# Optimization experiments

Measured on AMD Instinct MI355X. Metric: run time of the kernel, lower is better.

The kernel has to match this reference:

```python
import jax, jax.numpy as jnp
import numpy as np

N = 100000   # nodes
E = 1600000  # edges (avg degree 16)
F = 128      # num_features
H = 128      # hidden_channels
C = 8        # num_classes


def _gcn_conv(x, src, dst, W, b, num_nodes):
    """PyG GCNConv: add self-loops, symmetric normalization, linear-then-aggregate, +bias."""
    h = x @ W  # [N, out]
    loops = jnp.arange(num_nodes, dtype=src.dtype)
    s = jnp.concatenate([src, loops])
    d = jnp.concatenate([dst, loops])
    deg = jax.ops.segment_sum(jnp.ones_like(s, dtype=h.dtype), d, num_segments=num_nodes)
    dinv = jax.lax.rsqrt(jnp.maximum(deg, 1.0))  # deg >= 1 thanks to self-loops
    norm = dinv[s] * dinv[d]  # [E+N]
    out = jax.ops.segment_sum(h[s] * norm[:, None], d, num_segments=num_nodes)
    return out + b


def setup_inputs() -> dict:
    key = jax.random.key(0)
    k1, k2, k3, k4 = jax.random.split(key, 4)
    x = jax.random.normal(k1, (N, F), dtype=jnp.float32)
    edge_index = jax.random.randint(k2, (2, E), 0, N, dtype=jnp.int32)
    W1 = jax.random.normal(k3, (F, H), dtype=jnp.float32) * (1.0 / np.sqrt(F))
    b1 = jnp.zeros((H,), dtype=jnp.float32)
    W2 = jax.random.normal(k4, (H, C), dtype=jnp.float32) * (1.0 / np.sqrt(H))
    b2 = jnp.zeros((C,), dtype=jnp.float32)
    return {"x": x, "edge_index": edge_index, "W1": W1, "b1": b1, "W2": W2, "b2": b2}


def reference(x, edge_index, W1, b1, W2, b2):
    src, dst = edge_index[0], edge_index[1]
    h = _gcn_conv(x, src, dst, W1, b1, N)
    h = jax.nn.relu(h)
    out = _gcn_conv(h, src, dst, W2, b2, N)
    return out
```

## Files before the change

kernel.cpp:

```cpp
#include <hip/hip_runtime.h>
#include <hip/hip_bf16.h>
#include <hip/hip_fp16.h>

#define NN 100000
#define EE 1600000
#define FF 128
#define HH 128
#define CC 8

#define CH 4096
#define NBK ((NN + 511) / 512)
#define NCH ((EE + CH - 1) / CH)
#define HSZ (NBK * NCH)

typedef _Float16 half8 __attribute__((ext_vector_type(8)));
typedef float f32x4 __attribute__((ext_vector_type(4)));

__global__ __launch_bounds__(1024) void k_scan1(const int* __restrict__ in,
                                                int* __restrict__ outp,
                                                int* __restrict__ bsum, int n) {
  __shared__ int sh[1024];
  int t = threadIdx.x;
  int i = blockIdx.x * 1024 + t;
  int v = (i < n) ? in[i] : 0;
  sh[t] = v;
  __syncthreads();
  for (int offs = 1; offs < 1024; offs <<= 1) {
    int add = (t >= offs) ? sh[t - offs] : 0;
    __syncthreads();
    sh[t] += add;
    __syncthreads();
  }
  if (i < n) outp[i] = sh[t] - v;
  if (t == 1023) bsum[blockIdx.x] = sh[1023];
}

__global__ __launch_bounds__(128) void k_scan2(int* __restrict__ bsum, int nb) {
  __shared__ int sh[128];
  int t = threadIdx.x;
  int v = (t < nb) ? bsum[t] : 0;
  sh[t] = v;
  __syncthreads();
  for (int offs = 1; offs < 128; offs <<= 1) {
    int add = (t >= offs) ? sh[t - offs] : 0;
    __syncthreads();
    sh[t] += add;
    __syncthreads();
  }
  if (t < nb) bsum[t] = sh[t] - v;
}

__global__ __launch_bounds__(1024) void k_scan3(int* __restrict__ outp,
                                                const int* __restrict__ bsum,
                                                int n, int e) {
  int i = blockIdx.x * 1024 + threadIdx.x;
  if (i < n) outp[i] += bsum[blockIdx.x];
  if (i == 0) outp[n] = e;
}

__global__ __launch_bounds__(256) void k_histA(const int* __restrict__ dst,
                                               int* __restrict__ hist) {
  __shared__ int lh[NBK];
  int c = blockIdx.x, t = threadIdx.x;
  for (int b = t; b < NBK; b += 256) lh[b] = 0;
  __syncthreads();
  int e0 = c * CH, e1 = min(e0 + CH, EE);
  for (int j = e0 + t; j < e1; j += 256) atomicAdd(&lh[dst[j] >> 9], 1);
  __syncthreads();
  for (int b = t; b < NBK; b += 256) hist[b * NCH + c] = lh[b];
}

__global__ __launch_bounds__(256) void k_scatA(const int* __restrict__ src,
                                               const int* __restrict__ dst,
                                               const int* __restrict__ hoff,
                                               unsigned int* __restrict__ stage) {
  __shared__ int lcur[NBK];
  int c = blockIdx.x, t = threadIdx.x;
  for (int b = t; b < NBK; b += 256) lcur[b] = hoff[b * NCH + c];
  __syncthreads();
  int e0 = c * CH, e1 = min(e0 + CH, EE);
  for (int j = e0 + t; j < e1; j += 256) {
    int d = dst[j];
    int pos = atomicAdd(&lcur[d >> 9], 1);
    stage[pos] = (unsigned int)src[j] | ((unsigned int)(d & 511) << 17);
  }
}

__global__ __launch_bounds__(256) void k_bucketB(const unsigned int* __restrict__ stage,
                                                 const int* __restrict__ hoff,
                                                 int* __restrict__ col,
                                                 int* __restrict__ rowptr,
                                                 float* __restrict__ dinv) {
  __shared__ int lcnt[512];
  __shared__ int lpart[256];
  int b = blockIdx.x, t = threadIdx.x;
  int n0 = b * 512;
  lcnt[t] = 0;
  lcnt[t + 256] = 0;
  __syncthreads();
  int e0 = hoff[b * NCH];
  int e1 = hoff[(b + 1) * NCH];
  for (int j = e0 + t; j < e1; j += 256)
    atomicAdd(&lcnt[stage[j] >> 17], 1);
  __syncthreads();
  int c0 = lcnt[2 * t], c1 = lcnt[2 * t + 1];
  lpart[t] = c0 + c1;
  __syncthreads();
  for (int offs = 1; offs < 256; offs <<= 1) {
    int add = (t >= offs) ? lpart[t - offs] : 0;
    __syncthreads();
    lpart[t] += add;
    __syncthreads();
  }
  int base0 = e0 + lpart[t] - (c0 + c1);
  int base1 = base0 + c0;
  int node0 = n0 + 2 * t, node1 = n0 + 2 * t + 1;
  if (node0 <= NN) rowptr[node0] = base0;
  if (node1 <= NN) rowptr[node1] = base1;
  if (node0 < NN) dinv[node0] = rsqrtf((float)c0 + 1.f);
  if (node1 < NN) dinv[node1] = rsqrtf((float)c1 + 1.f);
  lcnt[2 * t] = base0;
  lcnt[2 * t + 1] = base1;
  __syncthreads();
  for (int j = e0 + t; j < e1; j += 256) {
    unsigned int v = stage[j];
    int pos = atomicAdd(&lcnt[v >> 17], 1);
    col[pos] = (int)(v & 0x1FFFFu);
  }
}

__global__ __launch_bounds__(256) void k_gemm1(const float* __restrict__ x,
                                               const float* __restrict__ W,
                                               __half* __restrict__ h, int n) {
  __shared__ _Float16 Wl[128 * 128];
  int t = threadIdx.x;
  {
    int c = t & 127;
    int kg0 = t >> 7;
    for (int kg = kg0; kg < 16; kg += 2) {
      _Float16 tmp[8];
#pragma unroll
      for (int j = 0; j < 8; ++j)
        tmp[j] = (_Float16)W[(size_t)(kg * 8 + j) * 128 + c];
      int byteoff = (c * 256 + kg * 16) ^ ((c & 7) << 4);
      *(half8*)((char*)Wl + byteoff) = *(half8*)tmp;
    }
  }
  __syncthreads();

  int row0 = blockIdx.x * 64;
  int w = t >> 6, l = t & 63;
  int rw = w >> 1, cw = w & 1;
  int lr = l & 15, g = l >> 4;

  f32x4 acc[2][4];
#pragma unroll
  for (int ar = 0; ar < 2; ++ar)
#pragma unroll
    for (int bt = 0; bt < 4; ++bt)
#pragma unroll
      for (int r = 0; r < 4; ++r) acc[ar][bt][r] = 0.f;

  for (int kt = 0; kt < 4; ++kt) {
    half8 a[2];
#pragma unroll
    for (int ar = 0; ar < 2; ++ar) {
      int row = row0 + rw * 32 + ar * 16 + lr;
      if (row < n) {
        const float* p = &x[(size_t)row * 128 + kt * 32 + g * 8];
        float4 v0 = *(const float4*)p;
        float4 v1 = *(const float4*)(p + 4);
        a[ar][0] = (_Float16)v0.x; a[ar][1] = (_Float16)v0.y;
        a[ar][2] = (_Float16)v0.z; a[ar][3] = (_Float16)v0.w;
        a[ar][4] = (_Float16)v1.x; a[ar][5] = (_Float16)v1.y;
        a[ar][6] = (_Float16)v1.z; a[ar][7] = (_Float16)v1.w;
      } else {
#pragma unroll
        for (int j = 0; j < 8; ++j) a[ar][j] = (_Float16)0.f;
      }
    }
#pragma unroll
    for (int bt = 0; bt < 4; ++bt) {
      int c = cw * 64 + bt * 16 + lr;
      int byteoff = (c * 256 + kt * 64 + g * 16) ^ ((c & 7) << 4);
      half8 bb = *(const half8*)((const char*)Wl + byteoff);
      acc[0][bt] = __builtin_amdgcn_mfma_f32_16x16x32_f16(a[0], bb, acc[0][bt], 0, 0, 0);
      acc[1][bt] = __builtin_amdgcn_mfma_f32_16x16x32_f16(a[1], bb, acc[1][bt], 0, 0, 0);
    }
  }

#pragma unroll
  for (int ar = 0; ar < 2; ++ar)
#pragma unroll
    for (int bt = 0; bt < 4; ++bt)
#pragma unroll
      for (int r = 0; r < 4; ++r) {
        int row = row0 + rw * 32 + ar * 16 + g * 4 + r;
        int c = cw * 64 + bt * 16 + lr;
        if (row < n) h[(size_t)row * 128 + c] = __float2half(acc[ar][bt][r]);
      }
}

__global__ __launch_bounds__(256) void k_agg1(const __half* __restrict__ h,
                                              const int* __restrict__ rowptr,
                                              const int* __restrict__ col,
                                              const float* __restrict__ dinv,
                                              const float* __restrict__ b1,
                                              __half2* __restrict__ out, int n) {
  int wid = threadIdx.x >> 6;
  int lane = threadIdx.x & 63;
  int node = blockIdx.x * 4 + wid;
  if (node >= n) return;
  float dn = dinv[node];
  const __half2* hp = (const __half2*)h;
  float2 acc = make_float2(0.f, 0.f);
  int e0 = rowptr[node], e1 = rowptr[node + 1];
  int e = e0;
  for (; e + 7 < e1; e += 8) {
    int s[8];
#pragma unroll
    for (int u = 0; u < 8; ++u) s[u] = col[e + u];
    float w[8];
    __half2 f[8];
#pragma unroll
    for (int u = 0; u < 8; ++u) w[u] = dinv[s[u]];
#pragma unroll
    for (int u = 0; u < 8; ++u) f[u] = hp[(size_t)s[u] * 64 + lane];
#pragma unroll
    for (int u = 0; u < 8; ++u) {
      float2 ff = __half22float2(f[u]);
      float ww = w[u] * dn;
      acc.x = fmaf(ww, ff.x, acc.x);
      acc.y = fmaf(ww, ff.y, acc.y);
    }
  }
  for (; e + 1 < e1; e += 2) {
    int s0 = col[e], s1 = col[e + 1];
    float w0 = dinv[s0] * dn, w1 = dinv[s1] * dn;
    float2 f0 = __half22float2(hp[(size_t)s0 * 64 + lane]);
    float2 f1 = __half22float2(hp[(size_t)s1 * 64 + lane]);
    acc.x = fmaf(w0, f0.x, acc.x); acc.y = fmaf(w0, f0.y, acc.y);
    acc.x = fmaf(w1, f1.x, acc.x); acc.y = fmaf(w1, f1.y, acc.y);
  }
  if (e < e1) {
    int s = col[e];
    float w = dinv[s] * dn;
    float2 f = __half22float2(hp[(size_t)s * 64 + lane]);
    acc.x = fmaf(w, f.x, acc.x);
    acc.y = fmaf(w, f.y, acc.y);
  }
  {
    float w = dn * dn;
    float2 f = __half22float2(hp[(size_t)node * 64 + lane]);
    acc.x = fmaf(w, f.x, acc.x);
    acc.y = fmaf(w, f.y, acc.y);
  }
  float2 bb = ((const float2*)b1)[lane];
  acc.x = fmaxf(acc.x + bb.x, 0.f);
  acc.y = fmaxf(acc.y + bb.y, 0.f);
  out[(size_t)node * 64 + lane] = __floats2half2_rn(acc.x, acc.y);
}

__global__ __launch_bounds__(256) void k_gemm2(const __half* __restrict__ a,
                                               const float* __restrict__ W2,
                                               __half* __restrict__ h2, int n) {
  int r = blockIdx.x * 256 + threadIdx.x;
  if (r >= n) return;
  float acc[8];
#pragma unroll
  for (int c = 0; c < 8; ++c) acc[c] = 0.f;
  const __half2* ap = (const __half2*)(a + (size_t)r * 128);
#pragma unroll 8
  for (int k2 = 0; k2 < 64; ++k2) {
    float2 v = __half22float2(ap[k2]);
    int k = k2 * 2;
#pragma unroll
    for (int c = 0; c < 8; ++c) {
      acc[c] = fmaf(v.x, W2[(k + 0) * 8 + c], acc[c]);
      acc[c] = fmaf(v.y, W2[(k + 1) * 8 + c], acc[c]);
    }
  }
  union { __half2 h2v[4]; uint2 u2[2]; } pk;
#pragma unroll
  for (int c = 0; c < 4; ++c)
    pk.h2v[c] = __floats2half2_rn(acc[2 * c], acc[2 * c + 1]);
  *(uint2*)&h2[(size_t)r * 8] = pk.u2[0];
  *(uint2*)&h2[(size_t)r * 8 + 4] = pk.u2[1];
}

__global__ __launch_bounds__(256) void k_agg2(const __half* __restrict__ h2,
                                              const int* __restrict__ rowptr,
                                              const int* __restrict__ col,
                                              const float* __restrict__ dinv,
                                              const float* __restrict__ b2,
                                              float* __restrict__ out, int n) {
  int gthread = blockIdx.x * 256 + threadIdx.x;
  int node = gthread >> 3, f = gthread & 7;
  if (node >= n) return;
  float dn = dinv[node];
  float acc = 0.f;
  int e0 = rowptr[node], e1 = rowptr[node + 1];
  int e = e0;
  for (; e + 3 < e1; e += 4) {
    int s0 = col[e], s1 = col[e + 1], s2 = col[e + 2], s3 = col[e + 3];
    float w0 = dinv[s0], w1 = dinv[s1], w2 = dinv[s2], w3 = dinv[s3];
    float v0 = __half2float(h2[(size_t)s0 * 8 + f]);
    float v1 = __half2float(h2[(size_t)s1 * 8 + f]);
    float v2 = __half2float(h2[(size_t)s2 * 8 + f]);
    float v3 = __half2float(h2[(size_t)s3 * 8 + f]);
    acc = fmaf(w0 * dn, v0, acc);
    acc = fmaf(w1 * dn, v1, acc);
    acc = fmaf(w2 * dn, v2, acc);
    acc = fmaf(w3 * dn, v3, acc);
  }
  for (; e < e1; ++e) {
    int s = col[e];
    acc = fmaf(dinv[s] * dn, __half2float(h2[(size_t)s * 8 + f]), acc);
  }
  acc = fmaf(dn * dn, __half2float(h2[(size_t)node * 8 + f]), acc);
  out[(size_t)node * 8 + f] = acc + b2[f];
}

extern "C" void kernel_launch(void* const* d_in, const int* in_sizes, int n_in,
                              void* d_out, int out_size, void* d_ws, size_t ws_size,
                              hipStream_t stream) {
  const float* x  = (const float*)d_in[0];
  const int* eidx = (const int*)d_in[1];
  const float* W1 = (const float*)d_in[2];
  const float* b1 = (const float*)d_in[3];
  const float* W2 = (const float*)d_in[4];
  const float* b2 = (const float*)d_in[5];
  float* out = (float*)d_out;
  const int* src = eidx;
  const int* dst = eidx + EE;

  char* ws = (char*)d_ws;
  size_t off = 0;
  auto alloc = [&](size_t bytes) -> char* {
    char* p = ws + off;
    off = (off + bytes + 255) & ~(size_t)255;
    return p;
  };

  float*        dinv   = (float*)       alloc((size_t)NN * 4);
  int*          rowptr = (int*)         alloc((size_t)(NN + 1) * 4);
  int*          bsum   = (int*)         alloc(1024 * 4);
  int*          hist_g = (int*)         alloc((size_t)HSZ * 4);
  int*          hist_s = (int*)         alloc((size_t)(HSZ + 1) * 4);
  unsigned int* stage  = (unsigned int*)alloc((size_t)EE * 4);
  int*          colbuf = (int*)         alloc((size_t)EE * 4);
  __half*       h1     = (__half*)      alloc((size_t)NN * HH * 2);
  __half2*      agg1   = (__half2*)     alloc((size_t)NN * HH * 2);
  __half*       h2     = (__half*)h1;

  int nbScanH = (HSZ + 1023) / 1024;

  k_histA<<<NCH, 256, 0, stream>>>(dst, hist_g);
  k_scan1<<<nbScanH, 1024, 0, stream>>>(hist_g, hist_s, bsum, HSZ);
  k_scan2<<<1, 128, 0, stream>>>(bsum, nbScanH);
  k_scan3<<<nbScanH, 1024, 0, stream>>>(hist_s, bsum, HSZ, EE);
  k_scatA<<<NCH, 256, 0, stream>>>(src, dst, hist_s, stage);
  k_bucketB<<<NBK, 256, 0, stream>>>(stage, hist_s, colbuf, rowptr, dinv);

  int nbG1 = (NN + 63) / 64;
  k_gemm1<<<nbG1, 256, 0, stream>>>(x, W1, h1, NN);
  k_agg1<<<(NN + 3) / 4, 256, 0, stream>>>(h1, rowptr, colbuf, dinv, b1, agg1, NN);

  int nbG2 = (NN + 255) / 256;
  k_gemm2<<<nbG2, 256, 0, stream>>>((const __half*)agg1, W2, h2, NN);
  k_agg2<<<(NN * 8 + 255) / 256, 256, 0, stream>>>(h2, rowptr, colbuf, dinv, b2, out, NN);
}
```

Baseline: 179.7 us.

## Fuse scatter with gemm1, fold gemm2 into agg1, use 256-node buckets

Folds the edge scatter pass into the first GEMM launch, with the first NCH blocks doing the scatter and the rest doing the GEMM, so the two independent stages overlap. Fuses the second linear layer into the first aggregation through a wave-wide shuffle reduction, which avoids writing and rereading the 128-wide intermediate. Bucket size drops to 256 nodes so bucketB maps one thread per node, and the scan grows to match. The trade-off is a longer shuffle-reduction tail for each node and a larger histogram.

```diff
diff --git a/kernel.cpp b/kernel.cpp
--- a/kernel.cpp
+++ b/kernel.cpp
@@ -9,7 +9,7 @@
 #define CC 8
 
 #define CH 4096
-#define NBK ((NN + 511) / 512)
+#define NBK ((NN + 255) / 256)
 #define NCH ((EE + CH - 1) / CH)
 #define HSZ (NBK * NCH)
 
@@ -35,13 +35,13 @@
   if (t == 1023) bsum[blockIdx.x] = sh[1023];
 }
 
-__global__ __launch_bounds__(128) void k_scan2(int* __restrict__ bsum, int nb) {
-  __shared__ int sh[128];
+__global__ __launch_bounds__(256) void k_scan2(int* __restrict__ bsum, int nb) {
+  __shared__ int sh[256];
   int t = threadIdx.x;
   int v = (t < nb) ? bsum[t] : 0;
   sh[t] = v;
   __syncthreads();
-  for (int offs = 1; offs < 128; offs <<= 1) {
+  for (int offs = 1; offs < 256; offs <<= 1) {
     int add = (t >= offs) ? sh[t - offs] : 0;
     __syncthreads();
     sh[t] += add;
@@ -65,75 +65,33 @@
   for (int b = t; b < NBK; b += 256) lh[b] = 0;
   __syncthreads();
   int e0 = c * CH, e1 = min(e0 + CH, EE);
-  for (int j = e0 + t; j < e1; j += 256) atomicAdd(&lh[dst[j] >> 9], 1);
+  for (int j = e0 + t; j < e1; j += 256) atomicAdd(&lh[dst[j] >> 8], 1);
   __syncthreads();
   for (int b = t; b < NBK; b += 256) hist[b * NCH + c] = lh[b];
 }
 
-__global__ __launch_bounds__(256) void k_scatA(const int* __restrict__ src,
-                                               const int* __restrict__ dst,
-                                               const int* __restrict__ hoff,
-                                               unsigned int* __restrict__ stage) {
-  __shared__ int lcur[NBK];
-  int c = blockIdx.x, t = threadIdx.x;
-  for (int b = t; b < NBK; b += 256) lcur[b] = hoff[b * NCH + c];
-  __syncthreads();
-  int e0 = c * CH, e1 = min(e0 + CH, EE);
-  for (int j = e0 + t; j < e1; j += 256) {
-    int d = dst[j];
-    int pos = atomicAdd(&lcur[d >> 9], 1);
-    stage[pos] = (unsigned int)src[j] | ((unsigned int)(d & 511) << 17);
-  }
-}
-
-__global__ __launch_bounds__(256) void k_bucketB(const unsigned int* __restrict__ stage,
-                                                 const int* __restrict__ hoff,
-                                                 int* __restrict__ col,
-                                                 int* __restrict__ rowptr,
-                                                 float* __restrict__ dinv) {
-  __shared__ int lcnt[512];
-  __shared__ int lpart[256];
-  int b = blockIdx.x, t = threadIdx.x;
-  int n0 = b * 512;
-  lcnt[t] = 0;
-  lcnt[t + 256] = 0;
-  __syncthreads();
-  int e0 = hoff[b * NCH];
-  int e1 = hoff[(b + 1) * NCH];
-  for (int j = e0 + t; j < e1; j += 256)
-    atomicAdd(&lcnt[stage[j] >> 17], 1);
-  __syncthreads();
-  int c0 = lcnt[2 * t], c1 = lcnt[2 * t + 1];
-  lpart[t] = c0 + c1;
-  __syncthreads();
-  for (int offs = 1; offs < 256; offs <<= 1) {
-    int add = (t >= offs) ? lpart[t - offs] : 0;
-    __syncthreads();
-    lpart[t] += add;
-    __syncthreads();
-  }
-  int base0 = e0 + lpart[t] - (c0 + c1);
-  int base1 = base0 + c0;
-  int node0 = n0 + 2 * t, node1 = n0 + 2 * t + 1;
-  if (node0 <= NN) rowptr[node0] = base0;
-  if (node1 <= NN) rowptr[node1] = base1;
-  if (node0 < NN) dinv[node0] = rsqrtf((float)c0 + 1.f);
-  if (node1 < NN) dinv[node1] = rsqrtf((float)c1 + 1.f);
-  lcnt[2 * t] = base0;
-  lcnt[2 * t + 1] = base1;
-  __syncthreads();
-  for (int j = e0 + t; j < e1; j += 256) {
-    unsigned int v = stage[j];
-    int pos = atomicAdd(&lcnt[v >> 17], 1);
-    col[pos] = (int)(v & 0x1FFFFu);
-  }
-}
-
-__global__ __launch_bounds__(256) void k_gemm1(const float* __restrict__ x,
-                                               const float* __restrict__ W,
-                                               __half* __restrict__ h, int n) {
+__global__ __launch_bounds__(256) void k_scat_gemm1(
+    const int* __restrict__ src, const int* __restrict__ dst,
+    const int* __restrict__ hoff, unsigned int* __restrict__ stage,
+    const float* __restrict__ x, const float* __restrict__ W,
+    __half* __restrict__ h, int n) {
   __shared__ _Float16 Wl[128 * 128];
   int t = threadIdx.x;
+
+  if (blockIdx.x < NCH) {
+    int* lcur = (int*)Wl;
+    int c = blockIdx.x;
+    for (int b = t; b < NBK; b += 256) lcur[b] = hoff[b * NCH + c];
+    __syncthreads();
+    int e0 = c * CH, e1 = min(e0 + CH, EE);
+    for (int j = e0 + t; j < e1; j += 256) {
+      int d = dst[j];
+      int pos = atomicAdd(&lcur[d >> 8], 1);
+      stage[pos] = (unsigned int)src[j] | ((unsigned int)(d & 255) << 17);
+    }
+    return;
+  }
+
   {
     int c = t & 127;
     int kg0 = t >> 7;
@@ -148,7 +106,7 @@
   }
   __syncthreads();
 
-  int row0 = blockIdx.x * 64;
+  int row0 = (blockIdx.x - NCH) * 64;
   int w = t >> 6, l = t & 63;
   int rw = w >> 1, cw = w & 1;
   int lr = l & 15, g = l >> 4;
@@ -201,16 +159,61 @@
       }
 }
 
-__global__ __launch_bounds__(256) void k_agg1(const __half* __restrict__ h,
-                                              const int* __restrict__ rowptr,
-                                              const int* __restrict__ col,
-                                              const float* __restrict__ dinv,
-                                              const float* __restrict__ b1,
-                                              __half2* __restrict__ out, int n) {
+__global__ __launch_bounds__(256) void k_bucketB(const unsigned int* __restrict__ stage,
+                                                 const int* __restrict__ hoff,
+                                                 int* __restrict__ col,
+                                                 int* __restrict__ rowptr,
+                                                 float* __restrict__ dinv) {
+  __shared__ int lcnt[256];
+  __shared__ int lpart[256];
+  int b = blockIdx.x, t = threadIdx.x;
+  int n0 = b * 256;
+  lcnt[t] = 0;
+  __syncthreads();
+  int e0 = hoff[b * NCH];
+  int e1 = hoff[(b + 1) * NCH];
+  for (int j = e0 + t; j < e1; j += 256)
+    atomicAdd(&lcnt[stage[j] >> 17], 1);
+  __syncthreads();
+  int c = lcnt[t];
+  lpart[t] = c;
+  __syncthreads();
+  for (int offs = 1; offs < 256; offs <<= 1) {
+    int add = (t >= offs) ? lpart[t - offs] : 0;
+    __syncthreads();
+    lpart[t] += add;
+    __syncthreads();
+  }
+  int base = e0 + lpart[t] - c;
+  int node = n0 + t;
+  if (node <= NN) rowptr[node] = base;
+  if (node < NN) dinv[node] = rsqrtf((float)c + 1.f);
+  __syncthreads();
+  lcnt[t] = base;
+  __syncthreads();
+  for (int j = e0 + t; j < e1; j += 256) {
+    unsigned int v = stage[j];
+    int pos = atomicAdd(&lcnt[v >> 17], 1);
+    col[pos] = (int)(v & 0x1FFFFu);
+  }
+}
+
+__global__ __launch_bounds__(256) void k_agg1f(const __half* __restrict__ h,
+                                               const int* __restrict__ rowptr,
+                                               const int* __restrict__ col,
+                                               const float* __restrict__ dinv,
+                                               const float* __restrict__ b1,
+                                               const float* __restrict__ W2,
+                                               __half* __restrict__ h2, int n) {
   int wid = threadIdx.x >> 6;
   int lane = threadIdx.x & 63;
   int node = blockIdx.x * 4 + wid;
   if (node >= n) return;
+  float4 wa0 = *(const float4*)&W2[(2 * lane) * 8];
+  float4 wa1 = *(const float4*)&W2[(2 * lane) * 8 + 4];
+  float4 wb0 = *(const float4*)&W2[(2 * lane + 1) * 8];
+  float4 wb1 = *(const float4*)&W2[(2 * lane + 1) * 8 + 4];
+
   float dn = dinv[node];
   const __half2* hp = (const __half2*)h;
   float2 acc = make_float2(0.f, 0.f);
@@ -258,34 +261,34 @@
   float2 bb = ((const float2*)b1)[lane];
   acc.x = fmaxf(acc.x + bb.x, 0.f);
   acc.y = fmaxf(acc.y + bb.y, 0.f);
-  out[(size_t)node * 64 + lane] = __floats2half2_rn(acc.x, acc.y);
-}
-
-__global__ __launch_bounds__(256) void k_gemm2(const __half* __restrict__ a,
-                                               const float* __restrict__ W2,
-                                               __half* __restrict__ h2, int n) {
-  int r = blockIdx.x * 256 + threadIdx.x;
-  if (r >= n) return;
-  float acc[8];
-#pragma unroll
-  for (int c = 0; c < 8; ++c) acc[c] = 0.f;
-  const __half2* ap = (const __half2*)(a + (size_t)r * 128);
-#pragma unroll 8
-  for (int k2 = 0; k2 < 64; ++k2) {
-    float2 v = __half22float2(ap[k2]);
-    int k = k2 * 2;
-#pragma unroll
-    for (int c = 0; c < 8; ++c) {
-      acc[c] = fmaf(v.x, W2[(k + 0) * 8 + c], acc[c]);
-      acc[c] = fmaf(v.y, W2[(k + 1) * 8 + c], acc[c]);
-    }
-  }
-  union { __half2 h2v[4]; uint2 u2[2]; } pk;
-#pragma unroll
-  for (int c = 0; c < 4; ++c)
-    pk.h2v[c] = __floats2half2_rn(acc[2 * c], acc[2 * c + 1]);
-  *(uint2*)&h2[(size_t)r * 8] = pk.u2[0];
-  *(uint2*)&h2[(size_t)r * 8 + 4] = pk.u2[1];
+
+  float p0 = acc.x * wa0.x + acc.y * wb0.x;
+  float p1 = acc.x * wa0.y + acc.y * wb0.y;
+  float p2 = acc.x * wa0.z + acc.y * wb0.z;
+  float p3 = acc.x * wa0.w + acc.y * wb0.w;
+  float p4 = acc.x * wa1.x + acc.y * wb1.x;
+  float p5 = acc.x * wa1.y + acc.y * wb1.y;
+  float p6 = acc.x * wa1.z + acc.y * wb1.z;
+  float p7 = acc.x * wa1.w + acc.y * wb1.w;
+#pragma unroll
+  for (int m = 1; m < 64; m <<= 1) {
+    p0 += __shfl_xor(p0, m);
+    p1 += __shfl_xor(p1, m);
+    p2 += __shfl_xor(p2, m);
+    p3 += __shfl_xor(p3, m);
+    p4 += __shfl_xor(p4, m);
+    p5 += __shfl_xor(p5, m);
+    p6 += __shfl_xor(p6, m);
+    p7 += __shfl_xor(p7, m);
+  }
+  if (lane == 0) {
+    union { __half2 hh[4]; uint4 u; } pk;
+    pk.hh[0] = __floats2half2_rn(p0, p1);
+    pk.hh[1] = __floats2half2_rn(p2, p3);
+    pk.hh[2] = __floats2half2_rn(p4, p5);
+    pk.hh[3] = __floats2half2_rn(p6, p7);
+    *(uint4*)&h2[(size_t)node * 8] = pk.u;
+  }
 }
 
 __global__ __launch_bounds__(256) void k_agg2(const __half* __restrict__ h2,
@@ -350,23 +353,22 @@
   unsigned int* stage  = (unsigned int*)alloc((size_t)EE * 4);
   int*          colbuf = (int*)         alloc((size_t)EE * 4);
   __half*       h1     = (__half*)      alloc((size_t)NN * HH * 2);
-  __half2*      agg1   = (__half2*)     alloc((size_t)NN * HH * 2);
-  __half*       h2     = (__half*)h1;
+  __half*       h2     = (__half*)      alloc((size_t)NN * CC * 2);
 
   int nbScanH = (HSZ + 1023) / 1024;
 
   k_histA<<<NCH, 256, 0, stream>>>(dst, hist_g);
   k_scan1<<<nbScanH, 1024, 0, stream>>>(hist_g, hist_s, bsum, HSZ);
-  k_scan2<<<1, 128, 0, stream>>>(bsum, nbScanH);
+  k_scan2<<<1, 256, 0, stream>>>(bsum, nbScanH);
   k_scan3<<<nbScanH, 1024, 0, stream>>>(hist_s, bsum, HSZ, EE);
-  k_scatA<<<NCH, 256, 0, stream>>>(src, dst, hist_s, stage);
+
+  int nbG1 = (NN + 63) / 64;
+  k_scat_gemm1<<<NCH + nbG1, 256, 0, stream>>>(src, dst, hist_s, stage,
+                                               x, W1, h1, NN);
   k_bucketB<<<NBK, 256, 0, stream>>>(stage, hist_s, colbuf, rowptr, dinv);
 
-  int nbG1 = (NN + 63) / 64;
-  k_gemm1<<<nbG1, 256, 0, stream>>>(x, W1, h1, NN);
-  k_agg1<<<(NN + 3) / 4, 256, 0, stream>>>(h1, rowptr, colbuf, dinv, b1, agg1, NN);
-
-  int nbG2 = (NN + 255) / 256;
-  k_gemm2<<<nbG2, 256, 0, stream>>>((const __half*)agg1, W2, h2, NN);
-  k_agg2<<<(NN * 8 + 255) / 256, 256, 0, stream>>>(h2, rowptr, colbuf, dinv, b2, out, NN);
-}
+  k_agg1f<<<(NN + 3) / 4, 256, 0, stream>>>(h1, rowptr, colbuf, dinv, b1, W2,
+                                            h2, NN);
+  k_agg2<<<(NN * 8 + 255) / 256, 256, 0, stream>>>(h2, rowptr, colbuf, dinv,
+                                                   b2, out, NN);
+}
```

New measurement: 176.3 us. About the same (-1.9%).
